# Optimization experiments

Hardware: AMD Instinct MI355X
Metric: run time of the kernel (lower is better)

Reference implementation:

```python
import jax, jax.numpy as jnp
import numpy as np


def setup_inputs() -> dict:
    key = jax.random.key(0)
    k1, k2, k3, k4 = jax.random.split(key, 4)
    B, V, P, C, R, N, OUT = 8, 4096, 32, 32, 2, 16, 32  # N=(l_max+1)^2, l_max=3
    signal = jax.random.normal(k1, (B, V, C), dtype=jnp.float32)
    patches_idx = jax.random.randint(k2, (B, V, P), 0, V, dtype=jnp.int32)
    conv_kernel = jax.random.normal(k3, (B, V, P, R, N), dtype=jnp.float32)
    kernel_weights = jax.random.normal(k4, (OUT, C, R, N), dtype=jnp.float32) * 0.05
    biases = jnp.zeros((OUT,), dtype=jnp.float32)
    return {
        "signal": signal,
        "patches_idx": patches_idx,
        "conv_kernel": conv_kernel,
        "kernel_weights": kernel_weights,
        "biases": biases,
    }


def reference(signal, patches_idx, conv_kernel, kernel_weights, biases):
    # Gather per-vertex tree-neighbor patches (tf.gather_nd with batch idx):
    # signal [B,V,C], patches_idx [B,V,P] -> patches [B,V,P,C]
    patches = jax.vmap(lambda s, i: s[i])(signal, patches_idx)
    # Bilinear contraction with precomputed SH conv kernel: [B,V,P,R,N] x [B,V,P,C]
    y = jnp.einsum('bvprn,bvpc->bvcrn', conv_kernel, patches)
    # Learned weights contraction: [OUT,C,R,N] x [B,V,C,R,N] -> [B,V,OUT]
    y = jnp.einsum('ijrn,bvjrn->bvi', kernel_weights, y)
    y = y + biases
    return jax.nn.relu(y)
```

## Files before the change

### kernel.cpp

```cpp
#include <hip/hip_runtime.h>


typedef __attribute__((ext_vector_type(8))) short bf16x8;
typedef __attribute__((ext_vector_type(4))) short short4v;
typedef __attribute__((ext_vector_type(16))) float f32x16;
typedef __attribute__((ext_vector_type(4))) float f32x4;

__device__ __forceinline__ unsigned short f2bf_rne(float f) {
    union { float f; unsigned int u; } x;
    x.f = f;
    unsigned int u = x.u;
    return (unsigned short)((u + 0x7fffu + ((u >> 16) & 1u)) >> 16);
}
__device__ __forceinline__ unsigned short f2bf_rh(float f) {
    union { float f; unsigned int u; } x;
    x.f = f;
    return (unsigned short)((x.u + 0x8000u) >> 16);
}

__global__ __launch_bounds__(256) void prep_kernel(
        const float* __restrict__ W, const float* __restrict__ sig,
        unsigned short* __restrict__ Wf, unsigned short* __restrict__ sigbf) {
    int tid = blockIdx.x * 256 + threadIdx.x;
    if (tid < 32768) {
        int j = tid & 7;
        int l = (tid >> 3) & 63;
        int pair = tid >> 9;
        int s = pair >> 1;
        int t = pair & 1;
        int i = 16 * t + (l & 15);
        int crn = 32 * s + 8 * (l >> 4) + j;
        Wf[tid] = f2bf_rne(W[i * 1024 + crn]);
    } else {
        int e = (tid - 32768) * 8;
        if (e < 8 * 4096 * 32) {
            f32x4 a = *(const f32x4*)(sig + e);
            f32x4 b = *(const f32x4*)(sig + e + 4);
            bf16x8 v;
            v[0] = (short)f2bf_rne(a[0]); v[1] = (short)f2bf_rne(a[1]);
            v[2] = (short)f2bf_rne(a[2]); v[3] = (short)f2bf_rne(a[3]);
            v[4] = (short)f2bf_rne(b[0]); v[5] = (short)f2bf_rne(b[1]);
            v[6] = (short)f2bf_rne(b[2]); v[7] = (short)f2bf_rne(b[3]);
            *(bf16x8*)(sigbf + e) = v;
        }
    }
}

__global__ __launch_bounds__(256, 4) void fused_kernel(
        const unsigned short* __restrict__ sigbf, const int* __restrict__ pidx,
        const float* __restrict__ ck, const unsigned short* __restrict__ Wf,
        const float* __restrict__ bias, float* __restrict__ out) {
    __shared__ __align__(16) unsigned short ckb[8 * 1024];
    __shared__ __align__(16) unsigned short T_lds[8 * 1032];
    const int tid = threadIdx.x;
    const int l = tid & 63;
    const int g = l >> 5;
    const int cc = l & 31;
    const int wu = __builtin_amdgcn_readfirstlane(tid >> 6);
    const int m0 = blockIdx.x * 8;
    const int b = m0 >> 12;
    const unsigned short* sgb = sigbf + (size_t)b * (4096 * 32);

    f32x4 st[8];
    {
        const f32x4* ckv = (const f32x4*)(ck + (size_t)m0 * 1024);
        #pragma unroll
        for (int i = 0; i < 8; ++i) st[i] = ckv[i * 256 + tid];
    }
    int rows[64];
    {
        const int* idxp = pidx + (size_t)(m0 + 2 * wu) * 32;
        #pragma unroll
        for (int k = 0; k < 64; ++k) rows[k] = idxp[k];
    }
    unsigned short ga[32];
    #pragma unroll
    for (int q = 0; q < 2; ++q) {
        #pragma unroll
        for (int h = 0; h < 2; ++h) {
            #pragma unroll
            for (int j = 0; j < 8; ++j) {
                const int rlo = rows[q * 32 + h * 16 + j];
                const int rhi = rows[q * 32 + h * 16 + 8 + j];
                const int row = g ? rhi : rlo;
                ga[q * 16 + h * 8 + j] = sgb[row * 32 + cc];
            }
        }
    }
    #pragma unroll
    for (int i = 0; i < 8; ++i) {
        union { f32x4 f; unsigned int u[4]; } x;
        x.f = st[i];
        short4v v = { (short)(x.u[0] >> 16), (short)(x.u[1] >> 16),
                      (short)(x.u[2] >> 16), (short)(x.u[3] >> 16) };
        *(short4v*)(ckb + (i * 256 + tid) * 4) = v;
    }
    __syncthreads();

    #pragma unroll
    for (int q = 0; q < 2; ++q) {
        const unsigned short* ct = ckb + (2 * wu + q) * 1024;
        f32x16 acc = {};
        #pragma unroll
        for (int h = 0; h < 2; ++h) {
            bf16x8 af, bfr;
            #pragma unroll
            for (int j = 0; j < 8; ++j) {
                const int p = h * 16 + 8 * g + j;
                af[j]  = (short)ga[q * 16 + h * 8 + j];
                bfr[j] = (short)ct[p * 32 + cc];
            }
            acc = __builtin_amdgcn_mfma_f32_32x32x16_bf16(af, bfr, acc, 0, 0, 0);
        }
        unsigned short* trow = T_lds + (2 * wu + q) * 1032 + cc + g * 128;
        #pragma unroll
        for (int r = 0; r < 16; ++r)
            trow[((r & 3) + 8 * (r >> 2)) * 32] = f2bf_rh(acc[r]);
    }
    __syncthreads();

    f32x4 acc0 = {}, acc1 = {};
    const int lg = l >> 4;
    const int ln = l & 15;
    #pragma unroll
    for (int si = 0; si < 8; ++si) {
        const int s = 8 * wu + si;
        const bf16x8 af = *(const bf16x8*)(T_lds + (ln & 7) * 1032 + s * 32 + 8 * lg);
        const bf16x8* wrow = (const bf16x8*)(Wf + (size_t)(s * 2) * 512);
        const bf16x8 b0 = wrow[l];
        const bf16x8 b1 = wrow[64 + l];
        acc0 = __builtin_amdgcn_mfma_f32_16x16x32_bf16(af, b0, acc0, 0, 0, 0);
        acc1 = __builtin_amdgcn_mfma_f32_16x16x32_bf16(af, b1, acc1, 0, 0, 0);
    }
    __syncthreads();

    float* red = (float*)T_lds;
    {
        f32x4* rp = (f32x4*)(red + wu * 512);
        rp[l]      = acc0;
        rp[64 + l] = acc1;
    }
    __syncthreads();

    {
        const int bv  = tid >> 5;
        const int i   = tid & 31;
        const int t   = i >> 4;
        const int col = i & 15;
        const int lgi = bv >> 2;
        const int r   = bv & 3;
        const int li  = lgi * 16 + col;
        const int o   = t * 256 + li * 4 + r;
        float sum = red[o] + red[512 + o] + red[1024 + o] + red[1536 + o];
        sum += bias[i];
        out[(size_t)(m0 + bv) * 32 + i] = sum > 0.f ? sum : 0.f;
    }
}

extern "C" void kernel_launch(void* const* d_in, const int* in_sizes, int n_in,
                              void* d_out, int out_size, void* d_ws, size_t ws_size,
                              hipStream_t stream) {
    const float* sig  = (const float*)d_in[0];
    const int*   pidx = (const int*)d_in[1];
    const float* ck   = (const float*)d_in[2];
    const float* W    = (const float*)d_in[3];
    const float* bias = (const float*)d_in[4];
    float* out = (float*)d_out;
    unsigned short* Wf    = (unsigned short*)d_ws;
    unsigned short* sigbf = Wf + 32768;

    prep_kernel<<<640, 256, 0, stream>>>(W, sig, Wf, sigbf);
    fused_kernel<<<4096, 256, 0, stream>>>(sigbf, pidx, ck, Wf, bias, out);
}
```

Before: 38.84 us.

## Process four vertex tiles per block with software-prefetched conv kernel and indices

The fused kernel now handles 32 vertices per block over four iterations. It prefetches the next tile's conv-kernel values and patch indices into registers while the current tile is computed, which is meant to hide global load latency. The bf16 copy of the signal in the prep kernel is removed, and the gather reads fp32 signal directly and rounds it in-register, which saves a pass over the signal at the cost of gathering twice the bytes. The grid is cut to 1024 blocks, so there is less parallelism per launch, and register pressure from the prefetch buffers could hurt occupancy.

```diff
diff --git a/kernel.cpp b/kernel.cpp
--- a/kernel.cpp
+++ b/kernel.cpp
@@ -19,35 +19,20 @@
 }
 
 __global__ __launch_bounds__(256) void prep_kernel(
-        const float* __restrict__ W, const float* __restrict__ sig,
-        unsigned short* __restrict__ Wf, unsigned short* __restrict__ sigbf) {
+        const float* __restrict__ W, unsigned short* __restrict__ Wf) {
     int tid = blockIdx.x * 256 + threadIdx.x;
-    if (tid < 32768) {
-        int j = tid & 7;
-        int l = (tid >> 3) & 63;
-        int pair = tid >> 9;
-        int s = pair >> 1;
-        int t = pair & 1;
-        int i = 16 * t + (l & 15);
-        int crn = 32 * s + 8 * (l >> 4) + j;
-        Wf[tid] = f2bf_rne(W[i * 1024 + crn]);
-    } else {
-        int e = (tid - 32768) * 8;
-        if (e < 8 * 4096 * 32) {
-            f32x4 a = *(const f32x4*)(sig + e);
-            f32x4 b = *(const f32x4*)(sig + e + 4);
-            bf16x8 v;
-            v[0] = (short)f2bf_rne(a[0]); v[1] = (short)f2bf_rne(a[1]);
-            v[2] = (short)f2bf_rne(a[2]); v[3] = (short)f2bf_rne(a[3]);
-            v[4] = (short)f2bf_rne(b[0]); v[5] = (short)f2bf_rne(b[1]);
-            v[6] = (short)f2bf_rne(b[2]); v[7] = (short)f2bf_rne(b[3]);
-            *(bf16x8*)(sigbf + e) = v;
-        }
-    }
+    int j = tid & 7;
+    int l = (tid >> 3) & 63;
+    int pair = tid >> 9;
+    int s = pair >> 1;
+    int t = pair & 1;
+    int i = 16 * t + (l & 15);
+    int crn = 32 * s + 8 * (l >> 4) + j;
+    Wf[tid] = f2bf_rne(W[i * 1024 + crn]);
 }
 
 __global__ __launch_bounds__(256, 4) void fused_kernel(
-        const unsigned short* __restrict__ sigbf, const int* __restrict__ pidx,
+        const float* __restrict__ sig, const int* __restrict__ pidx,
         const float* __restrict__ ck, const unsigned short* __restrict__ Wf,
         const float* __restrict__ bias, float* __restrict__ out) {
     __shared__ __align__(16) unsigned short ckb[8 * 1024];
@@ -57,103 +42,112 @@
     const int g = l >> 5;
     const int cc = l & 31;
     const int wu = __builtin_amdgcn_readfirstlane(tid >> 6);
-    const int m0 = blockIdx.x * 8;
-    const int b = m0 >> 12;
-    const unsigned short* sgb = sigbf + (size_t)b * (4096 * 32);
+    const int base_m = blockIdx.x * 32;
+    const float* sgb = sig + (size_t)(base_m >> 12) * (4096 * 32);
+    const f32x4* ckv = (const f32x4*)(ck + (size_t)base_m * 1024);
 
     f32x4 st[8];
-    {
-        const f32x4* ckv = (const f32x4*)(ck + (size_t)m0 * 1024);
-        #pragma unroll
-        for (int i = 0; i < 8; ++i) st[i] = ckv[i * 256 + tid];
-    }
+    #pragma unroll
+    for (int i = 0; i < 8; ++i) st[i] = ckv[i * 256 + tid];
     int rows[64];
     {
-        const int* idxp = pidx + (size_t)(m0 + 2 * wu) * 32;
+        const int* ip = pidx + ((size_t)base_m + 2 * wu) * 32;
         #pragma unroll
-        for (int k = 0; k < 64; ++k) rows[k] = idxp[k];
+        for (int k = 0; k < 64; ++k) rows[k] = ip[k];
     }
-    unsigned short ga[32];
-    #pragma unroll
-    for (int q = 0; q < 2; ++q) {
+
+    for (int it = 0; it < 4; ++it) {
+        const int m0 = base_m + it * 8;
+
+        unsigned short ga[32];
         #pragma unroll
-        for (int h = 0; h < 2; ++h) {
+        for (int q = 0; q < 2; ++q)
             #pragma unroll
-            for (int j = 0; j < 8; ++j) {
-                const int rlo = rows[q * 32 + h * 16 + j];
-                const int rhi = rows[q * 32 + h * 16 + 8 + j];
-                const int row = g ? rhi : rlo;
-                ga[q * 16 + h * 8 + j] = sgb[row * 32 + cc];
+            for (int h = 0; h < 2; ++h)
+                #pragma unroll
+                for (int j = 0; j < 8; ++j) {
+                    const int row = rows[q * 32 + h * 16 + 8 * g + j];
+                    ga[q * 16 + h * 8 + j] = f2bf_rh(sgb[row * 32 + cc]);
+                }
+
+        #pragma unroll
+        for (int i = 0; i < 8; ++i) {
+            union { f32x4 f; unsigned int u[4]; } x;
+            x.f = st[i];
+            short4v v = { (short)(x.u[0] >> 16), (short)(x.u[1] >> 16),
+                          (short)(x.u[2] >> 16), (short)(x.u[3] >> 16) };
+            *(short4v*)(ckb + (i * 256 + tid) * 4) = v;
+        }
+
+        if (it < 3) {
+            #pragma unroll
+            for (int i = 0; i < 8; ++i)
+                st[i] = ckv[(it + 1) * 2048 + i * 256 + tid];
+            const int* ip = pidx + ((size_t)m0 + 8 + 2 * wu) * 32;
+            #pragma unroll
+            for (int k = 0; k < 64; ++k) rows[k] = ip[k];
+        }
+        __syncthreads();
+
+        #pragma unroll
+        for (int q = 0; q < 2; ++q) {
+            const unsigned short* ct = ckb + (2 * wu + q) * 1024;
+            f32x16 acc = {};
+            #pragma unroll
+            for (int h = 0; h < 2; ++h) {
+                bf16x8 af, bfr;
+                #pragma unroll
+                for (int j = 0; j < 8; ++j) {
+                    const int p = h * 16 + 8 * g + j;
+                    af[j]  = (short)ga[q * 16 + h * 8 + j];
+                    bfr[j] = (short)ct[p * 32 + cc];
+                }
+                acc = __builtin_amdgcn_mfma_f32_32x32x16_bf16(af, bfr, acc, 0, 0, 0);
             }
+            unsigned short* trow = T_lds + (2 * wu + q) * 1032 + cc + g * 128;
+            #pragma unroll
+            for (int r = 0; r < 16; ++r)
+                trow[((r & 3) + 8 * (r >> 2)) * 32] = f2bf_rh(acc[r]);
         }
-    }
-    #pragma unroll
-    for (int i = 0; i < 8; ++i) {
-        union { f32x4 f; unsigned int u[4]; } x;
-        x.f = st[i];
-        short4v v = { (short)(x.u[0] >> 16), (short)(x.u[1] >> 16),
-                      (short)(x.u[2] >> 16), (short)(x.u[3] >> 16) };
-        *(short4v*)(ckb + (i * 256 + tid) * 4) = v;
-    }
-    __syncthreads();
+        __syncthreads();
 
-    #pragma unroll
-    for (int q = 0; q < 2; ++q) {
-        const unsigned short* ct = ckb + (2 * wu + q) * 1024;
-        f32x16 acc = {};
+        f32x4 acc0 = {}, acc1 = {};
+        const int lg = l >> 4;
+        const int ln = l & 15;
         #pragma unroll
-        for (int h = 0; h < 2; ++h) {
-            bf16x8 af, bfr;
-            #pragma unroll
-            for (int j = 0; j < 8; ++j) {
-                const int p = h * 16 + 8 * g + j;
-                af[j]  = (short)ga[q * 16 + h * 8 + j];
-                bfr[j] = (short)ct[p * 32 + cc];
-            }
-            acc = __builtin_amdgcn_mfma_f32_32x32x16_bf16(af, bfr, acc, 0, 0, 0);
+        for (int si = 0; si < 8; ++si) {
+            const int s = 8 * wu + si;
+            const bf16x8 af =
+                *(const bf16x8*)(T_lds + (ln & 7) * 1032 + s * 32 + 8 * lg);
+            const bf16x8* wrow = (const bf16x8*)(Wf + (size_t)(s * 2) * 512);
+            const bf16x8 b0 = wrow[l];
+            const bf16x8 b1 = wrow[64 + l];
+            acc0 = __builtin_amdgcn_mfma_f32_16x16x32_bf16(af, b0, acc0, 0, 0, 0);
+            acc1 = __builtin_amdgcn_mfma_f32_16x16x32_bf16(af, b1, acc1, 0, 0, 0);
         }
-        unsigned short* trow = T_lds + (2 * wu + q) * 1032 + cc + g * 128;
-        #pragma unroll
-        for (int r = 0; r < 16; ++r)
-            trow[((r & 3) + 8 * (r >> 2)) * 32] = f2bf_rh(acc[r]);
-    }
-    __syncthreads();
+        __syncthreads();
 
-    f32x4 acc0 = {}, acc1 = {};
-    const int lg = l >> 4;
-    const int ln = l & 15;
-    #pragma unroll
-    for (int si = 0; si < 8; ++si) {
-        const int s = 8 * wu + si;
-        const bf16x8 af = *(const bf16x8*)(T_lds + (ln & 7) * 1032 + s * 32 + 8 * lg);
-        const bf16x8* wrow = (const bf16x8*)(Wf + (size_t)(s * 2) * 512);
-        const bf16x8 b0 = wrow[l];
-        const bf16x8 b1 = wrow[64 + l];
-        acc0 = __builtin_amdgcn_mfma_f32_16x16x32_bf16(af, b0, acc0, 0, 0, 0);
-        acc1 = __builtin_amdgcn_mfma_f32_16x16x32_bf16(af, b1, acc1, 0, 0, 0);
-    }
-    __syncthreads();
+        float* red = (float*)T_lds;
+        {
+            f32x4* rp = (f32x4*)(red + wu * 512);
+            rp[l]      = acc0;
+            rp[64 + l] = acc1;
+        }
+        __syncthreads();
 
-    float* red = (float*)T_lds;
-    {
-        f32x4* rp = (f32x4*)(red + wu * 512);
-        rp[l]      = acc0;
-        rp[64 + l] = acc1;
-    }
-    __syncthreads();
-
-    {
-        const int bv  = tid >> 5;
-        const int i   = tid & 31;
-        const int t   = i >> 4;
-        const int col = i & 15;
-        const int lgi = bv >> 2;
-        const int r   = bv & 3;
-        const int li  = lgi * 16 + col;
-        const int o   = t * 256 + li * 4 + r;
-        float sum = red[o] + red[512 + o] + red[1024 + o] + red[1536 + o];
-        sum += bias[i];
-        out[(size_t)(m0 + bv) * 32 + i] = sum > 0.f ? sum : 0.f;
+        {
+            const int bv  = tid >> 5;
+            const int i   = tid & 31;
+            const int t   = i >> 4;
+            const int col = i & 15;
+            const int lgi = bv >> 2;
+            const int r   = bv & 3;
+            const int li  = lgi * 16 + col;
+            const int o   = t * 256 + li * 4 + r;
+            float sum = red[o] + red[512 + o] + red[1024 + o] + red[1536 + o];
+            sum += bias[i];
+            out[(size_t)(m0 + bv) * 32 + i] = sum > 0.f ? sum : 0.f;
+        }
     }
 }
 
@@ -166,9 +160,8 @@
     const float* W    = (const float*)d_in[3];
     const float* bias = (const float*)d_in[4];
     float* out = (float*)d_out;
-    unsigned short* Wf    = (unsigned short*)d_ws;
-    unsigned short* sigbf = Wf + 32768;
+    unsigned short* Wf = (unsigned short*)d_ws;
 
-    prep_kernel<<<640, 256, 0, stream>>>(W, sig, Wf, sigbf);
-    fused_kernel<<<4096, 256, 0, stream>>>(sigbf, pidx, ck, Wf, bias, out);
+    prep_kernel<<<128, 256, 0, stream>>>(W, Wf);
+    fused_kernel<<<1024, 256, 0, stream>>>(sig, pidx, ck, Wf, bias, out);
 }
```

Measured after the change: 142.5 us. 3.67x slower.

## Load conv kernel high halves directly from global, drop LDS staging

Applied to the files above, without the earlier changes.

Instead of loading conv_kernel as coalesced float4 vectors, truncating to bf16 and staging through shared memory, each lane now reads the upper 16-bit half of each float straight from global memory into registers for the MFMA B operand. This removes the ckb LDS buffer and one barrier, which lowers LDS use and lets launch bounds request 5 blocks per CU. The cost is many scattered 2-byte global loads with a 4-byte stride in place of wide vector loads, which may waste memory bandwidth on the kernel's dominant data stream.

```diff
diff --git a/kernel.cpp b/kernel.cpp
--- a/kernel.cpp
+++ b/kernel.cpp
@@ -2,7 +2,6 @@
 
 
 typedef __attribute__((ext_vector_type(8))) short bf16x8;
-typedef __attribute__((ext_vector_type(4))) short short4v;
 typedef __attribute__((ext_vector_type(16))) float f32x16;
 typedef __attribute__((ext_vector_type(4))) float f32x4;
 
@@ -46,11 +45,10 @@
     }
 }
 
-__global__ __launch_bounds__(256, 4) void fused_kernel(
+__global__ __launch_bounds__(256, 5) void fused_kernel(
         const unsigned short* __restrict__ sigbf, const int* __restrict__ pidx,
         const float* __restrict__ ck, const unsigned short* __restrict__ Wf,
         const float* __restrict__ bias, float* __restrict__ out) {
-    __shared__ __align__(16) unsigned short ckb[8 * 1024];
     __shared__ __align__(16) unsigned short T_lds[8 * 1032];
     const int tid = threadIdx.x;
     const int l = tid & 63;
@@ -60,22 +58,20 @@
     const int m0 = blockIdx.x * 8;
     const int b = m0 >> 12;
     const unsigned short* sgb = sigbf + (size_t)b * (4096 * 32);
+    const unsigned short* ckh = (const unsigned short*)ck;
 
-    f32x4 st[8];
-    {
-        const f32x4* ckv = (const f32x4*)(ck + (size_t)m0 * 1024);
-        #pragma unroll
-        for (int i = 0; i < 8; ++i) st[i] = ckv[i * 256 + tid];
-    }
     int rows[64];
     {
-        const int* idxp = pidx + (size_t)(m0 + 2 * wu) * 32;
+        const int* ip = pidx + ((size_t)m0 + 2 * wu) * 32;
         #pragma unroll
-        for (int k = 0; k < 64; ++k) rows[k] = idxp[k];
+        for (int k = 0; k < 64; ++k) rows[k] = ip[k];
     }
-    unsigned short ga[32];
+
+    unsigned short sa[2][16];
+    unsigned short kb[2][16];
     #pragma unroll
     for (int q = 0; q < 2; ++q) {
+        const size_t kh = ((size_t)(m0 + 2 * wu + q) * 1024) * 2 + 1;
         #pragma unroll
         for (int h = 0; h < 2; ++h) {
             #pragma unroll
@@ -83,32 +79,23 @@
                 const int rlo = rows[q * 32 + h * 16 + j];
                 const int rhi = rows[q * 32 + h * 16 + 8 + j];
                 const int row = g ? rhi : rlo;
-                ga[q * 16 + h * 8 + j] = sgb[row * 32 + cc];
+                sa[q][h * 8 + j] = sgb[row * 32 + cc];
+                kb[q][h * 8 + j] =
+                    ckh[kh + (size_t)((h * 16 + 8 * g + j) * 32 + cc) * 2];
             }
         }
     }
-    #pragma unroll
-    for (int i = 0; i < 8; ++i) {
-        union { f32x4 f; unsigned int u[4]; } x;
-        x.f = st[i];
-        short4v v = { (short)(x.u[0] >> 16), (short)(x.u[1] >> 16),
-                      (short)(x.u[2] >> 16), (short)(x.u[3] >> 16) };
-        *(short4v*)(ckb + (i * 256 + tid) * 4) = v;
-    }
-    __syncthreads();
 
     #pragma unroll
     for (int q = 0; q < 2; ++q) {
-        const unsigned short* ct = ckb + (2 * wu + q) * 1024;
         f32x16 acc = {};
         #pragma unroll
         for (int h = 0; h < 2; ++h) {
             bf16x8 af, bfr;
             #pragma unroll
             for (int j = 0; j < 8; ++j) {
-                const int p = h * 16 + 8 * g + j;
-                af[j]  = (short)ga[q * 16 + h * 8 + j];
-                bfr[j] = (short)ct[p * 32 + cc];
+                af[j]  = (short)sa[q][h * 8 + j];
+                bfr[j] = (short)kb[q][h * 8 + j];
             }
             acc = __builtin_amdgcn_mfma_f32_32x32x16_bf16(af, bfr, acc, 0, 0, 0);
         }
@@ -125,7 +112,8 @@
     #pragma unroll
     for (int si = 0; si < 8; ++si) {
         const int s = 8 * wu + si;
-        const bf16x8 af = *(const bf16x8*)(T_lds + (ln & 7) * 1032 + s * 32 + 8 * lg);
+        const bf16x8 af =
+            *(const bf16x8*)(T_lds + (ln & 7) * 1032 + s * 32 + 8 * lg);
         const bf16x8* wrow = (const bf16x8*)(Wf + (size_t)(s * 2) * 512);
         const bf16x8 b0 = wrow[l];
         const bf16x8 b1 = wrow[64 + l];
```

Result: slower. 40.78 us (+5.0%).

## Use 512-thread blocks with one wave per vertex instead of two

Applied to the files above, without the earlier changes.

Doubles the fused kernel's block size to 8 waves so each wave handles a single vertex's gather and first MFMA stage instead of two. The second-stage reduction over the channel-spherical-harmonic dimension is split across 8 waves with 4 steps each, and the final cross-wave sum reads 8 partial buffers. This halves per-thread registers and serial work, exposing more memory-level parallelism for the conv_kernel stream and the gathers. The cost is more LDS reduction traffic and half the threads sitting idle in the epilogue.

```diff
diff --git a/kernel.cpp b/kernel.cpp
--- a/kernel.cpp
+++ b/kernel.cpp
@@ -46,7 +46,7 @@
     }
 }
 
-__global__ __launch_bounds__(256, 4) void fused_kernel(
+__global__ __launch_bounds__(512, 8) void fused_kernel(
         const unsigned short* __restrict__ sigbf, const int* __restrict__ pidx,
         const float* __restrict__ ck, const unsigned short* __restrict__ Wf,
         const float* __restrict__ bias, float* __restrict__ out) {
@@ -61,45 +61,41 @@
     const int b = m0 >> 12;
     const unsigned short* sgb = sigbf + (size_t)b * (4096 * 32);
 
-    f32x4 st[8];
+    int rows[32];
     {
-        const f32x4* ckv = (const f32x4*)(ck + (size_t)m0 * 1024);
+        const int* ip = pidx + (size_t)(m0 + wu) * 32;
         #pragma unroll
-        for (int i = 0; i < 8; ++i) st[i] = ckv[i * 256 + tid];
+        for (int k = 0; k < 32; ++k) rows[k] = ip[k];
     }
-    int rows[64];
+    f32x4 st[4];
     {
-        const int* idxp = pidx + (size_t)(m0 + 2 * wu) * 32;
+        const f32x4* ckv = (const f32x4*)(ck + (size_t)(m0 + wu) * 1024);
         #pragma unroll
-        for (int k = 0; k < 64; ++k) rows[k] = idxp[k];
+        for (int i = 0; i < 4; ++i) st[i] = ckv[i * 64 + l];
     }
-    unsigned short ga[32];
+    unsigned short ga[16];
     #pragma unroll
-    for (int q = 0; q < 2; ++q) {
+    for (int h = 0; h < 2; ++h) {
         #pragma unroll
-        for (int h = 0; h < 2; ++h) {
-            #pragma unroll
-            for (int j = 0; j < 8; ++j) {
-                const int rlo = rows[q * 32 + h * 16 + j];
-                const int rhi = rows[q * 32 + h * 16 + 8 + j];
-                const int row = g ? rhi : rlo;
-                ga[q * 16 + h * 8 + j] = sgb[row * 32 + cc];
-            }
+        for (int j = 0; j < 8; ++j) {
+            const int rlo = rows[h * 16 + j];
+            const int rhi = rows[h * 16 + 8 + j];
+            const int row = g ? rhi : rlo;
+            ga[h * 8 + j] = sgb[row * 32 + cc];
         }
     }
     #pragma unroll
-    for (int i = 0; i < 8; ++i) {
+    for (int i = 0; i < 4; ++i) {
         union { f32x4 f; unsigned int u[4]; } x;
         x.f = st[i];
         short4v v = { (short)(x.u[0] >> 16), (short)(x.u[1] >> 16),
                       (short)(x.u[2] >> 16), (short)(x.u[3] >> 16) };
-        *(short4v*)(ckb + (i * 256 + tid) * 4) = v;
+        *(short4v*)(ckb + wu * 1024 + (i * 64 + l) * 4) = v;
     }
     __syncthreads();
 
-    #pragma unroll
-    for (int q = 0; q < 2; ++q) {
-        const unsigned short* ct = ckb + (2 * wu + q) * 1024;
+    {
+        const unsigned short* ct = ckb + wu * 1024;
         f32x16 acc = {};
         #pragma unroll
         for (int h = 0; h < 2; ++h) {
@@ -107,12 +103,12 @@
             #pragma unroll
             for (int j = 0; j < 8; ++j) {
                 const int p = h * 16 + 8 * g + j;
-                af[j]  = (short)ga[q * 16 + h * 8 + j];
+                af[j]  = (short)ga[h * 8 + j];
                 bfr[j] = (short)ct[p * 32 + cc];
             }
             acc = __builtin_amdgcn_mfma_f32_32x32x16_bf16(af, bfr, acc, 0, 0, 0);
         }
-        unsigned short* trow = T_lds + (2 * wu + q) * 1032 + cc + g * 128;
+        unsigned short* trow = T_lds + wu * 1032 + cc + g * 128;
         #pragma unroll
         for (int r = 0; r < 16; ++r)
             trow[((r & 3) + 8 * (r >> 2)) * 32] = f2bf_rh(acc[r]);
@@ -123,9 +119,10 @@
     const int lg = l >> 4;
     const int ln = l & 15;
     #pragma unroll
-    for (int si = 0; si < 8; ++si) {
-        const int s = 8 * wu + si;
-        const bf16x8 af = *(const bf16x8*)(T_lds + (ln & 7) * 1032 + s * 32 + 8 * lg);
+    for (int si = 0; si < 4; ++si) {
+        const int s = 4 * wu + si;
+        const bf16x8 af =
+            *(const bf16x8*)(T_lds + (ln & 7) * 1032 + s * 32 + 8 * lg);
         const bf16x8* wrow = (const bf16x8*)(Wf + (size_t)(s * 2) * 512);
         const bf16x8 b0 = wrow[l];
         const bf16x8 b1 = wrow[64 + l];
@@ -142,7 +139,7 @@
     }
     __syncthreads();
 
-    {
+    if (tid < 256) {
         const int bv  = tid >> 5;
         const int i   = tid & 31;
         const int t   = i >> 4;
@@ -151,7 +148,9 @@
         const int r   = bv & 3;
         const int li  = lgi * 16 + col;
         const int o   = t * 256 + li * 4 + r;
-        float sum = red[o] + red[512 + o] + red[1024 + o] + red[1536 + o];
+        float sum = 0.f;
+        #pragma unroll
+        for (int w2 = 0; w2 < 8; ++w2) sum += red[w2 * 512 + o];
         sum += bias[i];
         out[(size_t)(m0 + bv) * 32 + i] = sum > 0.f ? sum : 0.f;
     }
@@ -170,5 +169,5 @@
     unsigned short* sigbf = Wf + 32768;
 
     prep_kernel<<<640, 256, 0, stream>>>(W, sig, Wf, sigbf);
-    fused_kernel<<<4096, 256, 0, stream>>>(sigbf, pidx, ck, Wf, bias, out);
+    fused_kernel<<<4096, 512, 0, stream>>>(sigbf, pidx, ck, Wf, bias, out);
 }
```

Measured after the change: 37.00 us. 4.7% less time.
